# Kernel optimization log

Measured on AMD Instinct MI355X. Metric: run time of the kernel, lower is better.

## Reference

```python
import jax, jax.numpy as jnp
import numpy as np
import math

B = 2; SEQ = 4096; D_MODEL = 768; D_STATE = 128; D_CONV = 4; EXPAND = 2; HEAD_DIM = 64
D_INNER = EXPAND * D_MODEL; D_SSM = D_INNER; NH = D_SSM // HEAD_DIM  # 24 heads
CONV_DIM = D_SSM + 2 * D_STATE; CHUNK = 256
D_IN_PROJ = 2 * D_INNER + 2 * D_STATE + NH


def causal_conv1d(x, w, b):
    # x: [B, C, L]; w: [C, W] depthwise kernel; left-pad for causality; silu activation
    W = w.shape[-1]; L = x.shape[-1]
    xp = jnp.pad(x, ((0, 0), (0, 0), (W - 1, 0)))
    y = b[None, :, None] + sum(xp[:, :, k:k + L] * w[None, :, k, None] for k in range(W))
    return jax.nn.silu(y)


def segsum(a):
    # a: [..., S] -> [..., S, S]; entry (i,j) = sum_{k=j+1..i} a_k for i>=j, -inf above diag
    S = a.shape[-1]
    cs = jnp.cumsum(a, -1)
    d = cs[..., :, None] - cs[..., None, :]
    mask = jnp.tril(jnp.ones((S, S), bool))
    return jnp.where(mask, d, -jnp.inf)


def ssd_chunk_scan(x, dt, A, Bm, Cm, Dp, chunk):
    # Mamba2 SSD chunked selective scan. x:[b,l,h,p] dt:[b,l,h] A:[h] Bm,Cm:[b,l,n] Dp:[h]
    b, l, h, p = x.shape; n = Bm.shape[-1]; nc = l // chunk
    xc = x.reshape(b, nc, chunk, h, p)
    Bc = Bm.reshape(b, nc, chunk, n)
    Cc = Cm.reshape(b, nc, chunk, n)
    dtc = dt.reshape(b, nc, chunk, h)
    a = jnp.transpose(A[None, None, None, :] * dtc, (0, 3, 1, 2))  # [b,h,c,s]
    Acs = jnp.cumsum(a, -1)
    Lm = jnp.exp(segsum(a))  # [b,h,c,s,s] lower-triangular decay
    # intra-chunk (diagonal block) outputs
    Ydiag = jnp.einsum('bcsn,bczn,bhcsz,bczh,bczhp->bcshp', Cc, Bc, Lm, dtc, xc)
    # per-chunk end states
    decay_states = jnp.exp(Acs[..., -1:] - Acs)  # [b,h,c,s]
    states = jnp.einsum('bczn,bhcz,bczh,bczhp->bchpn', Bc, decay_states, dtc, xc)
    # inter-chunk recurrence over nc chunks (small) via scan
    decay_chunk = jnp.exp(Acs[..., -1])  # [b,h,c]
    def step(hcar, inp):
        dcy, st = inp
        return dcy[..., None, None] * hcar + st, hcar  # emit state entering chunk
    _, prev = jax.lax.scan(step, jnp.zeros_like(states[:, 0]),
                           (jnp.moveaxis(decay_chunk, -1, 0), jnp.moveaxis(states, 1, 0)))
    prev = jnp.moveaxis(prev, 0, 1)  # [b,c,h,p,n]
    Yoff = jnp.einsum('bcsn,bchpn,bhcs->bcshp', Cc, prev, jnp.exp(Acs))
    return (Ydiag + Yoff).reshape(b, l, h, p) + Dp[None, None, :, None] * x


def _forward(u, time_diff, W_in, b_in, conv_w, conv_b, tconv1_w, tconv1_b,
             tconv2_w, tconv2_b, mlp_w1, mlp_b1, mlp_w2, mlp_b2, gate_w, gate_b,
             ln_w, ln_b, A_log, dt_bias, Dp, norm_w, W_out, b_out):
    silu = jax.nn.silu
    zxbcdt = u @ W_in.T + b_in  # [B,L,d_in_proj], d_mlp=0
    z = zxbcdt[..., :D_SSM]
    xBC = zxbcdt[..., D_SSM:D_SSM + CONV_DIM]
    dt = zxbcdt[..., D_SSM + CONV_DIM:]  # [B,L,H]
    A = -jnp.exp(A_log)
    xBC = jnp.transpose(causal_conv1d(jnp.transpose(xBC, (0, 2, 1)), conv_w, conv_b), (0, 2, 1))
    # time-gated dt path (time_diff: [B,H,L])
    ts = silu(time_diff @ mlp_w1.T + mlp_b1) @ mlp_w2.T + mlp_b2
    tdt = ts * time_diff
    tdt = causal_conv1d(tdt, tconv1_w, tconv1_b)
    tdt = causal_conv1d(tdt, tconv2_w, tconv2_b)  # [B,H,L]
    final_dt = dt * jnp.transpose(tdt, (0, 2, 1))
    x = xBC[..., :D_SSM]
    Bm = xBC[..., D_SSM:D_SSM + D_STATE]
    Cm = xBC[..., D_SSM + D_STATE:]
    dt_sp = jax.nn.softplus(final_dt + dt_bias)
    xh = x.reshape(x.shape[0], x.shape[1], NH, HEAD_DIM)
    y = ssd_chunk_scan(xh, dt_sp, A, Bm, Cm, Dp, CHUNK).reshape(x.shape[0], x.shape[1], D_SSM)
    # gated RMSNorm (norm_before_gate=False): gate first, then normalize
    yg = y * silu(z)
    y = yg * jax.lax.rsqrt(jnp.mean(yg * yg, -1, keepdims=True) + 1e-12) * norm_w
    out = y @ W_out.T + b_out
    # time residual gate + LayerNorm over seq_len
    tg = jax.nn.sigmoid(time_diff @ gate_w.T + gate_b)  # [B,H,1]
    tmix = tg * time_diff + (1.0 - tg) * tdt
    mu = jnp.mean(tmix, -1, keepdims=True)
    var = jnp.mean((tmix - mu) ** 2, -1, keepdims=True)
    time_out = (tmix - mu) * jax.lax.rsqrt(var + 1e-12) * ln_w + ln_b
    return out, time_out


def setup_inputs():
    key = jax.random.key(0)
    ks = jax.random.split(key, 16)
    def nrm(k, shape, scale=0.02):
        return jax.random.normal(k, shape, jnp.float32) * scale
    dtv = jnp.exp(jax.random.uniform(ks[10], (NH,), jnp.float32) * (math.log(0.1) - math.log(0.001)) + math.log(0.001))
    dtv = jnp.clip(dtv, 1e-4)
    dt_bias = dtv + jnp.log(-jnp.expm1(-dtv))
    A_log = jnp.log(jax.random.uniform(ks[11], (NH,), jnp.float32, 1.0, 16.0))
    return dict(
        u=jax.random.normal(ks[0], (B, SEQ, D_MODEL), jnp.float32),
        time_diff=jax.random.uniform(ks[1], (B, NH, SEQ), jnp.float32),
        W_in=nrm(ks[2], (D_IN_PROJ, D_MODEL)), b_in=jnp.zeros((D_IN_PROJ,), jnp.float32),
        conv_w=nrm(ks[3], (CONV_DIM, D_CONV), 0.2), conv_b=jnp.zeros((CONV_DIM,), jnp.float32),
        tconv1_w=nrm(ks[4], (NH, D_CONV), 0.2), tconv1_b=jnp.zeros((NH,), jnp.float32),
        tconv2_w=nrm(ks[5], (NH, D_CONV), 0.2), tconv2_b=jnp.zeros((NH,), jnp.float32),
        mlp_w1=nrm(ks[6], (SEQ, SEQ)), mlp_b1=jnp.zeros((SEQ,), jnp.float32),
        mlp_w2=nrm(ks[7], (SEQ, SEQ)), mlp_b2=jnp.zeros((SEQ,), jnp.float32),
        gate_w=nrm(ks[8], (1, SEQ)), gate_b=jnp.zeros((1,), jnp.float32),
        ln_w=jnp.ones((SEQ,), jnp.float32), ln_b=jnp.zeros((SEQ,), jnp.float32),
        A_log=A_log, dt_bias=dt_bias, Dp=jnp.ones((NH,), jnp.float32),
        norm_w=jnp.ones((D_SSM,), jnp.float32),
        W_out=nrm(ks[9], (D_MODEL, D_INNER)), b_out=jnp.zeros((D_MODEL,), jnp.float32),
    )


def reference(u, time_diff, W_in, b_in, conv_w, conv_b, tconv1_w, tconv1_b,
              tconv2_w, tconv2_b, mlp_w1, mlp_b1, mlp_w2, mlp_b2, gate_w, gate_b,
              ln_w, ln_b, A_log, dt_bias, Dp, norm_w, W_out, b_out):
    return _forward(u, time_diff, W_in, b_in, conv_w, conv_b, tconv1_w, tconv1_b,
                    tconv2_w, tconv2_b, mlp_w1, mlp_b1, mlp_w2, mlp_b2, gate_w, gate_b,
                    ln_w, ln_b, A_log, dt_bias, Dp, norm_w, W_out, b_out)
```

## Files before the change

kernel.cpp:

```cpp
#include <hip/hip_runtime.h>
#include <math.h>

#define BB 2
#define SEQ 4096
#define DMODEL 768
#define DSTATE 128
#define NHH 24
#define HDIM 64
#define DSSM 1536
#define CDIM 1792
#define CHK 256
#define NC 16
#define DPROJ 3352
#define MR (BB*SEQ)
#define KSPLIT 32
#define XSTR 1920
#define CT 16
#define SXS 270
#define STS 134

typedef __attribute__((ext_vector_type(8))) short bf16x8;
typedef __attribute__((ext_vector_type(8))) unsigned short u16x8;
typedef __attribute__((ext_vector_type(4))) float f32x4;

__device__ __forceinline__ float siluf(float x) { return x / (1.0f + expf(-x)); }

__device__ __forceinline__ unsigned short f2bf(float f) {
    unsigned u = __float_as_uint(f);
    unsigned r = (u + 0x7fffu + ((u >> 16) & 1u)) >> 16;
    return (unsigned short)r;
}

__device__ __forceinline__ float bf2f(unsigned short u) {
    return __uint_as_float(((unsigned)u) << 16);
}

__device__ __forceinline__ float4 bf2f4(ushort4 v) {
    float4 o;
    o.x = bf2f(v.x); o.y = bf2f(v.y); o.z = bf2f(v.z); o.w = bf2f(v.w);
    return o;
}

__device__ __forceinline__ void gload_lds16(const void* g, void* l) {
    __builtin_amdgcn_global_load_lds((const __attribute__((address_space(1))) unsigned int*)g,
                                     (__attribute__((address_space(3))) unsigned int*)l, 16, 0, 0);
}

__global__ __launch_bounds__(256) void cvt_bf16_k(const float* __restrict__ in,
    unsigned short* __restrict__ out, int n_valid, int n_total)
{
    int i = (blockIdx.x * 256 + threadIdx.x) * 4;
    if (i >= n_total) return;
    ushort4 o;
    if (i + 3 < n_valid) {
        float4 v = *(const float4*)&in[i];
        o.x = f2bf(v.x); o.y = f2bf(v.y); o.z = f2bf(v.z); o.w = f2bf(v.w);
    } else {
        o.x = (i + 0 < n_valid) ? f2bf(in[i + 0]) : 0;
        o.y = (i + 1 < n_valid) ? f2bf(in[i + 1]) : 0;
        o.z = (i + 2 < n_valid) ? f2bf(in[i + 2]) : 0;
        o.w = (i + 3 < n_valid) ? f2bf(in[i + 3]) : 0;
    }
    *(ushort4*)&out[i] = o;
}

__global__ __launch_bounds__(256) void gemm_mfma_nt(
    const unsigned short* __restrict__ A, const unsigned short* __restrict__ B,
    const float* __restrict__ bias, void* __restrict__ C, int N, int K, int KT,
    int nbias, int store_bf16, int NT)
{
    __shared__ unsigned short SMEM[16384];
    const int tid = threadIdx.x;
    const int w = tid >> 6, l = tid & 63;
    const int wr = w >> 1, wc = w & 1;
    const int lr = l & 15, lk = l >> 4;
    int nwg = gridDim.x, bid = blockIdx.x;
    int wg = (nwg & 7) ? bid : ((bid & 7) * (nwg >> 3) + (bid >> 3));
    const int m0 = (wg / NT) * 128, n0 = (wg % NT) * 128;
    f32x4 acc[4][4] = {};
    const int i16 = w * 64 + l;
    const int row0 = i16 >> 2, sl = i16 & 3;
    const size_t ga0 = (size_t)(m0 + row0) * K + sl * 8;
    const size_t ga1 = (size_t)(m0 + row0 + 64) * K + sl * 8;
    const size_t gb0 = (size_t)(n0 + row0) * K + sl * 8;
    const size_t gb1 = (size_t)(n0 + row0 + 64) * K + sl * 8;
    const int lo0 = (w * 64) * 8;
    const int lo1 = (256 + w * 64) * 8;

#define STAGE(bb, kt) { int ko = (kt) * 32;                                  \
      gload_lds16(A + ga0 + ko, &SMEM[(bb) * 4096 + lo0]);                   \
      gload_lds16(A + ga1 + ko, &SMEM[(bb) * 4096 + lo1]);                   \
      gload_lds16(B + gb0 + ko, &SMEM[8192 + (bb) * 4096 + lo0]);            \
      gload_lds16(B + gb1 + ko, &SMEM[8192 + (bb) * 4096 + lo1]); }

    STAGE(0, 0);
    for (int kt = 0; kt < KT; ++kt) {
        int cur = kt & 1;
        asm volatile("s_waitcnt vmcnt(0)" ::: "memory");
        __syncthreads();
        if (kt + 1 < KT) STAGE(cur ^ 1, kt + 1);
        bf16x8 af[4], bg[4];
#pragma unroll
        for (int mi = 0; mi < 4; ++mi)
            af[mi] = *(const bf16x8*)&SMEM[cur * 4096 + (wr * 64 + mi * 16 + lr) * 32 + lk * 8];
#pragma unroll
        for (int nj = 0; nj < 4; ++nj)
            bg[nj] = *(const bf16x8*)&SMEM[8192 + cur * 4096 + (wc * 64 + nj * 16 + lr) * 32 + lk * 8];
#pragma unroll
        for (int mi = 0; mi < 4; ++mi)
#pragma unroll
            for (int nj = 0; nj < 4; ++nj)
                acc[mi][nj] = __builtin_amdgcn_mfma_f32_16x16x32_bf16(af[mi], bg[nj], acc[mi][nj], 0, 0, 0);
    }
#undef STAGE
    if (store_bf16) {
        unsigned short* CL = SMEM;
#pragma unroll
        for (int half = 0; half < 2; ++half) {
            __syncthreads();
            if (wr == half) {
#pragma unroll
                for (int nj = 0; nj < 4; ++nj) {
                    int col = n0 + wc * 64 + nj * 16 + lr;
                    float bz = (col < nbias) ? bias[col] : 0.f;
                    int cl = wc * 64 + nj * 16 + lr;
#pragma unroll
                    for (int mi = 0; mi < 4; ++mi)
#pragma unroll
                        for (int r = 0; r < 4; ++r)
                            CL[(mi * 16 + lk * 4 + r) * 136 + cl] = f2bf(acc[mi][nj][r] + bz);
                }
            }
            __syncthreads();
            for (int i = tid; i < 1024; i += 256) {
                int rr = i >> 4, c8 = (i & 15) * 8;
                int m = m0 + half * 64 + rr;
                *(u16x8*)&((unsigned short*)C)[(size_t)m * N + n0 + c8] = *(const u16x8*)&CL[rr * 136 + c8];
            }
        }
    } else {
#pragma unroll
        for (int nj = 0; nj < 4; ++nj) {
            int col = n0 + wc * 64 + nj * 16 + lr;
            float bz = (col < nbias) ? bias[col] : 0.f;
#pragma unroll
            for (int mi = 0; mi < 4; ++mi) {
#pragma unroll
                for (int r = 0; r < 4; ++r) {
                    int m = m0 + wr * 64 + mi * 16 + lk * 4 + r;
                    ((float*)C)[(size_t)m * N + col] = acc[mi][nj][r] + bz;
                }
            }
        }
    }
}

__global__ __launch_bounds__(256) void gemm_mfma_dual(
    const unsigned short* __restrict__ A,
    const unsigned short* __restrict__ B1, const float* __restrict__ bias1,
    unsigned short* __restrict__ C1, int N1, int NT1, int nbias1, int NWG1,
    const unsigned short* __restrict__ B2, const float* __restrict__ bias2,
    unsigned short* __restrict__ C2, int N2, int NT2, int nbias2,
    int K, int KT)
{
    __shared__ unsigned short SMEM[16384];
    const int tid = threadIdx.x;
    const int w = tid >> 6, l = tid & 63;
    const int wr = w >> 1, wc = w & 1;
    const int lr = l & 15, lk = l >> 4;
    int nwg = gridDim.x, bid = blockIdx.x;
    int wg = (nwg & 7) ? bid : ((bid & 7) * (nwg >> 3) + (bid >> 3));
    const unsigned short* B;
    const float* bias;
    unsigned short* C;
    int N, NT, nbias;
    if (wg < NWG1) { B = B1; bias = bias1; C = C1; N = N1; NT = NT1; nbias = nbias1; }
    else { wg -= NWG1; B = B2; bias = bias2; C = C2; N = N2; NT = NT2; nbias = nbias2; }
    const int m0 = (wg / NT) * 128, n0 = (wg % NT) * 128;
    f32x4 acc[4][4] = {};
    const int i16 = w * 64 + l;
    const int row0 = i16 >> 2, sl = i16 & 3;
    const size_t ga0 = (size_t)(m0 + row0) * K + sl * 8;
    const size_t ga1 = (size_t)(m0 + row0 + 64) * K + sl * 8;
    const size_t gb0 = (size_t)(n0 + row0) * K + sl * 8;
    const size_t gb1 = (size_t)(n0 + row0 + 64) * K + sl * 8;
    const int lo0 = (w * 64) * 8;
    const int lo1 = (256 + w * 64) * 8;

#define STAGE(bb, kt) { int ko = (kt) * 32;                                  \
      gload_lds16(A + ga0 + ko, &SMEM[(bb) * 4096 + lo0]);                   \
      gload_lds16(A + ga1 + ko, &SMEM[(bb) * 4096 + lo1]);                   \
      gload_lds16(B + gb0 + ko, &SMEM[8192 + (bb) * 4096 + lo0]);            \
      gload_lds16(B + gb1 + ko, &SMEM[8192 + (bb) * 4096 + lo1]); }

    STAGE(0, 0);
    for (int kt = 0; kt < KT; ++kt) {
        int cur = kt & 1;
        asm volatile("s_waitcnt vmcnt(0)" ::: "memory");
        __syncthreads();
        if (kt + 1 < KT) STAGE(cur ^ 1, kt + 1);
        bf16x8 af[4], bg[4];
#pragma unroll
        for (int mi = 0; mi < 4; ++mi)
            af[mi] = *(const bf16x8*)&SMEM[cur * 4096 + (wr * 64 + mi * 16 + lr) * 32 + lk * 8];
#pragma unroll
        for (int nj = 0; nj < 4; ++nj)
            bg[nj] = *(const bf16x8*)&SMEM[8192 + cur * 4096 + (wc * 64 + nj * 16 + lr) * 32 + lk * 8];
#pragma unroll
        for (int mi = 0; mi < 4; ++mi)
#pragma unroll
            for (int nj = 0; nj < 4; ++nj)
                acc[mi][nj] = __builtin_amdgcn_mfma_f32_16x16x32_bf16(af[mi], bg[nj], acc[mi][nj], 0, 0, 0);
    }
#undef STAGE
    {
        unsigned short* CL = SMEM;
#pragma unroll
        for (int half = 0; half < 2; ++half) {
            __syncthreads();
            if (wr == half) {
#pragma unroll
                for (int nj = 0; nj < 4; ++nj) {
                    int col = n0 + wc * 64 + nj * 16 + lr;
                    float bz = (col < nbias) ? bias[col] : 0.f;
                    int cl = wc * 64 + nj * 16 + lr;
#pragma unroll
                    for (int mi = 0; mi < 4; ++mi)
#pragma unroll
                        for (int r = 0; r < 4; ++r)
                            CL[(mi * 16 + lk * 4 + r) * 136 + cl] = f2bf(acc[mi][nj][r] + bz);
                }
            }
            __syncthreads();
            for (int i = tid; i < 1024; i += 256) {
                int rr = i >> 4, c8 = (i & 15) * 8;
                int m = m0 + half * 64 + rr;
                *(u16x8*)&C[(size_t)m * N + n0 + c8] = *(const u16x8*)&CL[rr * 136 + c8];
            }
        }
    }
}

__global__ __launch_bounds__(256) void gemm_skinny_nt(const float* __restrict__ A,
    const float* __restrict__ Bw, float* __restrict__ part, int N, int K)
{
    __shared__ float sA[48 * 33];
    __shared__ float sB[128 * 33];
    const int nb = blockIdx.x, kb = blockIdx.y;
    const int n0 = nb * 128;
    const int KS = K / KSPLIT;
    const int k0 = kb * KS;
    const int tid = threadIdx.x;
    const int tx = tid & 31, ty = tid >> 5;
    float acc[6][4] = {{0.f}};
    for (int kc = 0; kc < KS; kc += 32) {
        if (kc) __syncthreads();
        for (int i = tid; i < 384; i += 256) {
            int m = i >> 3, k4 = (i & 7) * 4;
            float4 v = *(const float4*)&A[(size_t)m * K + k0 + kc + k4];
            sA[m * 33 + k4 + 0] = v.x;
            sA[m * 33 + k4 + 1] = v.y;
            sA[m * 33 + k4 + 2] = v.z;
            sA[m * 33 + k4 + 3] = v.w;
        }
        for (int i = tid; i < 1024; i += 256) {
            int n = i >> 3, k4 = (i & 7) * 4;
            float4 v = *(const float4*)&Bw[(size_t)(n0 + n) * K + k0 + kc + k4];
            sB[n * 33 + k4 + 0] = v.x;
            sB[n * 33 + k4 + 1] = v.y;
            sB[n * 33 + k4 + 2] = v.z;
            sB[n * 33 + k4 + 3] = v.w;
        }
        __syncthreads();
#pragma unroll 8
        for (int kk = 0; kk < 32; ++kk) {
            float a[6], b[4];
#pragma unroll
            for (int r = 0; r < 6; ++r) a[r] = sA[(ty * 6 + r) * 33 + kk];
#pragma unroll
            for (int j = 0; j < 4; ++j) b[j] = sB[(tx + j * 32) * 33 + kk];
#pragma unroll
            for (int r = 0; r < 6; ++r)
#pragma unroll
                for (int j = 0; j < 4; ++j)
                    acc[r][j] = fmaf(a[r], b[j], acc[r][j]);
        }
    }
    float* pb = part + (size_t)kb * 48 * N;
#pragma unroll
    for (int r = 0; r < 6; ++r)
#pragma unroll
        for (int j = 0; j < 4; ++j)
            pb[(size_t)(ty * 6 + r) * N + n0 + tx + j * 32] = acc[r][j];
}

__global__ __launch_bounds__(256) void reduce_part_k(const float* __restrict__ part,
    const float* __restrict__ bias, float* __restrict__ out, int N, int act)
{
    int idx = blockIdx.x * 256 + threadIdx.x;
    if (idx >= 48 * N) return;
    int n = idx % N;
    float s = bias[n];
#pragma unroll
    for (int kb = 0; kb < KSPLIT; ++kb) s += part[(size_t)kb * 48 * N + idx];
    if (act) s = siluf(s);
    out[idx] = s;
}

__global__ __launch_bounds__(256) void conv_xbc_k(const unsigned short* __restrict__ xbc,
    const float* __restrict__ cw, const float* __restrict__ cb,
    unsigned short* __restrict__ out)
{
    int idx = blockIdx.x * 256 + threadIdx.x;
    if (idx >= 448 * (MR / CT)) return;
    int slot = idx % 448;
    int g = idx / 448;
    int c4 = slot * 4;
    int b = g / (SEQ / CT);
    int t0 = (g % (SEQ / CT)) * CT;
    size_t rb = (size_t)b * SEQ;
    float4 cw0 = *(const float4*)&cw[(c4 + 0) * 4];
    float4 cw1 = *(const float4*)&cw[(c4 + 1) * 4];
    float4 cw2 = *(const float4*)&cw[(c4 + 2) * 4];
    float4 cw3 = *(const float4*)&cw[(c4 + 3) * 4];
    float4 cbv = *(const float4*)&cb[c4];
    float4 zero = {0.f, 0.f, 0.f, 0.f};
    float4 w0, w1, w2;
    w0 = (t0 - 3 >= 0) ? bf2f4(*(const ushort4*)&xbc[(rb + t0 - 3) * XSTR + c4]) : zero;
    w1 = (t0 - 2 >= 0) ? bf2f4(*(const ushort4*)&xbc[(rb + t0 - 2) * XSTR + c4]) : zero;
    w2 = (t0 - 1 >= 0) ? bf2f4(*(const ushort4*)&xbc[(rb + t0 - 1) * XSTR + c4]) : zero;
#pragma unroll
    for (int i = 0; i < CT; ++i) {
        int t = t0 + i;
        float4 w3 = bf2f4(*(const ushort4*)&xbc[(rb + t) * XSTR + c4]);
        float a0 = cbv.x + w0.x * cw0.x + w1.x * cw0.y + w2.x * cw0.z + w3.x * cw0.w;
        float a1 = cbv.y + w0.y * cw1.x + w1.y * cw1.y + w2.y * cw1.z + w3.y * cw1.w;
        float a2 = cbv.z + w0.z * cw2.x + w1.z * cw2.y + w2.z * cw2.z + w3.z * cw2.w;
        float a3 = cbv.w + w0.w * cw3.x + w1.w * cw3.y + w2.w * cw3.z + w3.w * cw3.w;
        ushort4 o;
        o.x = f2bf(siluf(a0)); o.y = f2bf(siluf(a1));
        o.z = f2bf(siluf(a2)); o.w = f2bf(siluf(a3));
        *(ushort4*)&out[(rb + t) * CDIM + c4] = o;
        w0 = w1; w1 = w2; w2 = w3;
    }
}

__global__ __launch_bounds__(256) void time_conv_k(const float* __restrict__ ts,
    const float* __restrict__ td, const float* __restrict__ w1, const float* __restrict__ b1,
    const float* __restrict__ w2, const float* __restrict__ b2, float* __restrict__ tdt)
{
    __shared__ float u0[SEQ];
    __shared__ float u1[SEQ];
    int row = blockIdx.x, h = row % NHH;
    const float* tsr = ts + (size_t)row * SEQ;
    const float* tdr = td + (size_t)row * SEQ;
    for (int i = threadIdx.x; i < SEQ; i += 256) u0[i] = tsr[i] * tdr[i];
    __syncthreads();
    float wa[4], wb[4];
#pragma unroll
    for (int k = 0; k < 4; ++k) { wa[k] = w1[h * 4 + k]; wb[k] = w2[h * 4 + k]; }
    float ba = b1[h], bbv = b2[h];
    for (int i = threadIdx.x; i < SEQ; i += 256) {
        float acc = ba;
#pragma unroll
        for (int k = 0; k < 4; ++k) { int tt = i + k - 3; if (tt >= 0) acc = fmaf(u0[tt], wa[k], acc); }
        u1[i] = siluf(acc);
    }
    __syncthreads();
    for (int i = threadIdx.x; i < SEQ; i += 256) {
        float acc = bbv;
#pragma unroll
        for (int k = 0; k < 4; ++k) { int tt = i + k - 3; if (tt >= 0) acc = fmaf(u1[tt], wb[k], acc); }
        tdt[(size_t)row * SEQ + i] = siluf(acc);
    }
}

__global__ __launch_bounds__(256) void dtsp_cum_k(const unsigned short* __restrict__ r1,
    const float* __restrict__ tdt, const float* __restrict__ dt_bias,
    const float* __restrict__ A_log, float* __restrict__ dtp, float* __restrict__ acs)
{
    __shared__ float wsum[4];
    int blk = blockIdx.x;
    int c = blk % NC;
    int bh = blk / NC;
    int h = bh % NHH, b = bh / NHH;
    int tid = threadIdx.x;
    int s = c * CHK + tid;
    size_t base = (size_t)bh * SEQ + s;
    float x = bf2f(r1[((size_t)(b * SEQ + s)) * XSTR + CDIM + h]) * tdt[base] + dt_bias[h];
    float dt = (x > 20.0f) ? x : log1pf(expf(x));
    dtp[base] = dt;
    float Ah = -expf(A_log[h]);
    float v = Ah * dt;
    int ln = tid & 63;
#pragma unroll
    for (int off = 1; off < 64; off <<= 1) {
        float t = __shfl_up(v, off, 64);
        if (ln >= off) v += t;
    }
    if (ln == 63) wsum[tid >> 6] = v;
    __syncthreads();
    float add = 0.f;
    int wv = tid >> 6;
#pragma unroll
    for (int i = 0; i < 3; ++i)
        if (i < wv) add += wsum[i];
    acs[base] = v + add;
}

__global__ __launch_bounds__(256) void ssd_states_sraw_k(const unsigned short* __restrict__ xc,
    const float* __restrict__ dtp, const float* __restrict__ acs_g,
    float* __restrict__ st, unsigned short* __restrict__ sraw)
{
    __shared__ float s_coef[256];
    __shared__ unsigned short SXT[64 * STS];
    __shared__ unsigned short SBT[128 * STS];
    int bid = blockIdx.x;
    int blk = (gridDim.x & 7) ? bid : ((bid & 7) * (gridDim.x >> 3) + (bid >> 3));
    int tid = threadIdx.x;
    int w = tid >> 6, l = tid & 63;
    int lr = l & 15, lk = l >> 4;
    if (blk >= BB * NC * NHH) {
        int t = blk - BB * NC * NHH;
        int bc = t / 10, tile = t % 10;
        int rem = tile, st_i = 0;
        for (st_i = 0; ; ++st_i) { if (rem < st_i + 1) break; rem -= st_i + 1; }
        int zt = rem;
// ... 199 lines not shown
            for (int r = 0; r < 4; ++r) {
                float es = esw[mi][r];
#pragma unroll
                for (int nj = 0; nj < 2; ++nj)
                    acc[mi][nj][r] += es * tmp[mi][nj][r];
            }
    }
    {
        f32x4 tmp[4][2] = {};
#pragma unroll
        for (int kt = 0; kt < 4; ++kt) {
            bf16x8 av[4], bv[2];
#pragma unroll
            for (int mi = 0; mi < 4; ++mi)
                av[mi] = *(const bf16x8*)&xc[(rowbase + w * 64 + mi * 16 + lr) * CDIM + DSSM + DSTATE + kt * 32 + lk * 8];
#pragma unroll
            for (int nj = 0; nj < 2; ++nj)
                bv[nj] = *(const bf16x8*)&pvbase[(pbase + nj * 16 + lr) * DSTATE + kt * 32 + lk * 8];
#pragma unroll
            for (int mi = 0; mi < 4; ++mi)
#pragma unroll
                for (int nj = 0; nj < 2; ++nj)
                    tmp[mi][nj] = __builtin_amdgcn_mfma_f32_16x16x32_bf16(av[mi], bv[nj], tmp[mi][nj], 0, 0, 0);
        }
        float eoff = expf(az0w);
#pragma unroll
        for (int mi = 0; mi < 4; ++mi)
#pragma unroll
            for (int r = 0; r < 4; ++r) {
                float es = esw[mi][r] * eoff;
#pragma unroll
                for (int nj = 0; nj < 2; ++nj)
                    acc[mi][nj][r] += es * tmp[mi][nj][r];
            }
    }
    float dph = Dp[h];
#pragma unroll
    for (int mi = 0; mi < 4; ++mi) {
#pragma unroll
        for (int r = 0; r < 4; ++r) {
            int s = w * 64 + mi * 16 + lk * 4 + r;
#pragma unroll
            for (int nj = 0; nj < 2; ++nj) {
                int p = pbase + nj * 16 + lr;
                float xv = bf2f(xc[(rowbase + s) * CDIM + h * HDIM + p]);
                Ybf[(rowbase + s) * DSSM + h * HDIM + p] = f2bf(acc[mi][nj][r] + dph * xv);
            }
        }
    }
}

__global__ __launch_bounds__(256) void rmsnorm_k(const unsigned short* __restrict__ Ybf_in,
    const unsigned short* __restrict__ zbf, const float* __restrict__ nw,
    unsigned short* __restrict__ Ybf_out)
{
    __shared__ float red[8];
    int row = blockIdx.x;
    const unsigned short* y = Ybf_in + (size_t)row * DSSM;
    const unsigned short* z = zbf + (size_t)row * DSSM;
    float v[6];
    float ss = 0.f;
#pragma unroll
    for (int k = 0; k < 6; ++k) {
        int i = threadIdx.x + k * 256;
        float g = bf2f(y[i]) * siluf(bf2f(z[i]));
        v[k] = g;
        ss = fmaf(g, g, ss);
    }
#pragma unroll
    for (int o = 32; o > 0; o >>= 1) ss += __shfl_down(ss, o, 64);
    int wv = threadIdx.x >> 6, ln = threadIdx.x & 63;
    if (ln == 0) red[wv] = ss;
    __syncthreads();
    float tot = red[0] + red[1] + red[2] + red[3];
    float sc = rsqrtf(tot / (float)DSSM + 1e-12f);
    unsigned short* yo = Ybf_out + (size_t)row * DSSM;
#pragma unroll
    for (int k = 0; k < 6; ++k) {
        int i = threadIdx.x + k * 256;
        yo[i] = f2bf(v[k] * sc * nw[i]);
    }
}

__global__ __launch_bounds__(256) void timeout_k(const float* __restrict__ td,
    const float* __restrict__ tdt, const float* __restrict__ gw, const float* __restrict__ gb,
    const float* __restrict__ lnw, const float* __restrict__ lnb, float* __restrict__ out2)
{
    __shared__ float tm[SEQ];
    __shared__ float red[8];
    int row = blockIdx.x;
    const float* tdr = td + (size_t)row * SEQ;
    const float* tdtr = tdt + (size_t)row * SEQ;
    int wv = threadIdx.x >> 6, ln = threadIdx.x & 63;
    float part = 0.f;
    for (int i = threadIdx.x; i < SEQ; i += 256) part = fmaf(tdr[i], gw[i], part);
#pragma unroll
    for (int o = 32; o > 0; o >>= 1) part += __shfl_down(part, o, 64);
    if (ln == 0) red[wv] = part;
    __syncthreads();
    float dot = red[0] + red[1] + red[2] + red[3];
    float tg = 1.f / (1.f + expf(-(dot + gb[0])));
    __syncthreads();
    float sum = 0.f;
    for (int i = threadIdx.x; i < SEQ; i += 256) {
        float x = tg * tdr[i] + (1.f - tg) * tdtr[i];
        tm[i] = x;
        sum += x;
    }
#pragma unroll
    for (int o = 32; o > 0; o >>= 1) sum += __shfl_down(sum, o, 64);
    if (ln == 0) red[wv] = sum;
    __syncthreads();
    float mu = (red[0] + red[1] + red[2] + red[3]) / (float)SEQ;
    __syncthreads();
    float s2 = 0.f;
    for (int i = threadIdx.x; i < SEQ; i += 256) { float d = tm[i] - mu; s2 = fmaf(d, d, s2); }
#pragma unroll
    for (int o = 32; o > 0; o >>= 1) s2 += __shfl_down(s2, o, 64);
    if (ln == 0) red[wv] = s2;
    __syncthreads();
    float var = (red[0] + red[1] + red[2] + red[3]) / (float)SEQ;
    float inv = rsqrtf(var + 1e-12f);
    for (int i = threadIdx.x; i < SEQ; i += 256)
        out2[(size_t)row * SEQ + i] = (tm[i] - mu) * inv * lnw[i] + lnb[i];
}

extern "C" void kernel_launch(void* const* d_in, const int* in_sizes, int n_in,
                              void* d_out, int out_size, void* d_ws, size_t ws_size,
                              hipStream_t stream)
{
    const float* u      = (const float*)d_in[0];
    const float* td     = (const float*)d_in[1];
    const float* W_in   = (const float*)d_in[2];
    const float* b_in   = (const float*)d_in[3];
    const float* conv_w = (const float*)d_in[4];
    const float* conv_b = (const float*)d_in[5];
    const float* t1w    = (const float*)d_in[6];
    const float* t1b    = (const float*)d_in[7];
    const float* t2w    = (const float*)d_in[8];
    const float* t2b    = (const float*)d_in[9];
    const float* m1w    = (const float*)d_in[10];
    const float* m1b    = (const float*)d_in[11];
    const float* m2w    = (const float*)d_in[12];
    const float* m2b    = (const float*)d_in[13];
    const float* gw     = (const float*)d_in[14];
    const float* gb     = (const float*)d_in[15];
    const float* lnw    = (const float*)d_in[16];
    const float* lnb    = (const float*)d_in[17];
    const float* A_log  = (const float*)d_in[18];
    const float* dt_bias= (const float*)d_in[19];
    const float* Dpv    = (const float*)d_in[20];
    const float* nw     = (const float*)d_in[21];
    const float* W_out  = (const float*)d_in[22];
    const float* b_out  = (const float*)d_in[23];
    float* out  = (float*)d_out;
    float* out2 = out + (size_t)MR * DMODEL;

    float* ws = (float*)d_ws;
    size_t o = 0;
    float* zbuf  = ws + o; o += (size_t)MR * DSSM;
    float* r1    = ws + o; o += (size_t)MR * DSSM;
    float* xcv   = ws + o; o += (size_t)MR * CDIM / 2;
    float* hid   = ws + o; o += (size_t)BB * NHH * SEQ;
    float* tss   = ws + o; o += (size_t)BB * NHH * SEQ;
    float* tdt   = ws + o; o += (size_t)BB * NHH * SEQ;
    float* dtp   = ws + o; o += (size_t)MR * NHH;
    float* acs_g = ws + o; o += (size_t)MR * NHH;
    float* pvb   = ws + o; o += (size_t)BB * NC * NHH * HDIM * DSTATE;
    unsigned short* sraw = (unsigned short*)(ws + o); o += (size_t)BB * NC * 16 * 4096 / 2;
    unsigned short* r1b = (unsigned short*)r1;
    float* stb = r1;
    unsigned short* ybf16 = (unsigned short*)r1;
    float* partb = xcv;
    unsigned short* xcv_bf = (unsigned short*)xcv;
    unsigned short* u_bf  = (unsigned short*)pvb;
    unsigned short* Wi_bf = (unsigned short*)(pvb + 3145728);
    unsigned short* pv16  = (unsigned short*)pvb;
    unsigned short* zbf   = (unsigned short*)zbuf;
    unsigned short* Y_bf  = (unsigned short*)xcv;
    unsigned short* Wo_bf = (unsigned short*)(zbuf + 6291456);

    dim3 blk(256);
    gemm_skinny_nt<<<dim3(SEQ / 128, KSPLIT), blk, 0, stream>>>(td, m1w, partb, SEQ, SEQ);
    reduce_part_k<<<dim3((48 * SEQ + 255) / 256), blk, 0, stream>>>(partb, m1b, hid, SEQ, 1);
    gemm_skinny_nt<<<dim3(SEQ / 128, KSPLIT), blk, 0, stream>>>(hid, m2w, partb, SEQ, SEQ);
    reduce_part_k<<<dim3((48 * SEQ + 255) / 256), blk, 0, stream>>>(partb, m2b, tss, SEQ, 0);
    time_conv_k<<<dim3(BB * NHH), blk, 0, stream>>>(tss, td, t1w, t1b, t2w, t2b, tdt);
    cvt_bf16_k<<<dim3((MR * DMODEL / 4 + 255) / 256), blk, 0, stream>>>(u, u_bf, MR * DMODEL, MR * DMODEL);
    cvt_bf16_k<<<dim3((3456 * DMODEL / 4 + 255) / 256), blk, 0, stream>>>(W_in, Wi_bf, DPROJ * DMODEL, 3456 * DMODEL);
    gemm_mfma_dual<<<dim3((XSTR / 128) * (MR / 128) + (DSSM / 128) * (MR / 128)), blk, 0, stream>>>(
        u_bf,
        Wi_bf + (size_t)DSSM * DMODEL, b_in + DSSM, r1b, XSTR, XSTR / 128, DPROJ - DSSM, (XSTR / 128) * (MR / 128),
        Wi_bf, b_in, zbf, DSSM, DSSM / 128, DSSM,
        DMODEL, DMODEL / 32);
    conv_xbc_k<<<dim3((448 * (MR / CT) + 255) / 256), blk, 0, stream>>>(r1b, conv_w, conv_b, xcv_bf);
    dtsp_cum_k<<<dim3(BB * NHH * NC), blk, 0, stream>>>(r1b, tdt, dt_bias, A_log, dtp, acs_g);
    ssd_states_sraw_k<<<dim3(BB * NC * NHH + BB * NC * 10), blk, 0, stream>>>(xcv_bf, dtp, acs_g, stb, sraw);
    ssd_scan_k<<<dim3(BB * NHH), blk, 0, stream>>>(stb, acs_g, pv16);
    ssd_y2_k<<<dim3(BB * NC * NHH * 2), blk, 0, stream>>>(xcv_bf, dtp, acs_g, sraw, pv16, Dpv, ybf16);
    rmsnorm_k<<<dim3(MR), blk, 0, stream>>>(ybf16, zbf, nw, Y_bf);
    cvt_bf16_k<<<dim3((DMODEL * DSSM / 4 + 255) / 256), blk, 0, stream>>>(W_out, Wo_bf, DMODEL * DSSM, DMODEL * DSSM);
    gemm_mfma_nt<<<dim3((DMODEL / 128) * (MR / 128)), blk, 0, stream>>>(
        Y_bf, Wo_bf, b_out, out, DMODEL, DSSM, DSSM / 32, DMODEL, 0, DMODEL / 128);
    timeout_k<<<dim3(BB * NHH), blk, 0, stream>>>(td, tdt, gw, gb, lnw, lnb, out2);
}
```

Measured before the change: 377.7 us.

## Merge independent kernels into shared launches to overlap skinny MLP GEMMs

The first skinny time-MLP GEMM now runs as extra workgroups inside the dual input-projection GEMM launch. The second skinny GEMM is merged into the causal conv launch, and the timeout LayerNorm rows are merged into the output GEMM launch. The partial-sum buffer moves to its own workspace region so it no longer aliases xcv. The intent is to overlap small, under-occupying kernels with larger ones and cut launch count. The cost is larger shared-memory allocations for some blocks and heterogeneous blocks within one grid.

```diff
diff --git a/kernel.cpp b/kernel.cpp
--- a/kernel.cpp
+++ b/kernel.cpp
@@ -64,112 +64,71 @@
     *(ushort4*)&out[i] = o;
 }
 
-__global__ __launch_bounds__(256) void gemm_mfma_nt(
-    const unsigned short* __restrict__ A, const unsigned short* __restrict__ B,
-    const float* __restrict__ bias, void* __restrict__ C, int N, int K, int KT,
-    int nbias, int store_bf16, int NT)
-{
-    __shared__ unsigned short SMEM[16384];
-    const int tid = threadIdx.x;
-    const int w = tid >> 6, l = tid & 63;
-    const int wr = w >> 1, wc = w & 1;
-    const int lr = l & 15, lk = l >> 4;
-    int nwg = gridDim.x, bid = blockIdx.x;
-    int wg = (nwg & 7) ? bid : ((bid & 7) * (nwg >> 3) + (bid >> 3));
-    const int m0 = (wg / NT) * 128, n0 = (wg % NT) * 128;
-    f32x4 acc[4][4] = {};
-    const int i16 = w * 64 + l;
-    const int row0 = i16 >> 2, sl = i16 & 3;
-    const size_t ga0 = (size_t)(m0 + row0) * K + sl * 8;
-    const size_t ga1 = (size_t)(m0 + row0 + 64) * K + sl * 8;
-    const size_t gb0 = (size_t)(n0 + row0) * K + sl * 8;
-    const size_t gb1 = (size_t)(n0 + row0 + 64) * K + sl * 8;
-    const int lo0 = (w * 64) * 8;
-    const int lo1 = (256 + w * 64) * 8;
-
-#define STAGE(bb, kt) { int ko = (kt) * 32;                                  \
-      gload_lds16(A + ga0 + ko, &SMEM[(bb) * 4096 + lo0]);                   \
-      gload_lds16(A + ga1 + ko, &SMEM[(bb) * 4096 + lo1]);                   \
-      gload_lds16(B + gb0 + ko, &SMEM[8192 + (bb) * 4096 + lo0]);            \
-      gload_lds16(B + gb1 + ko, &SMEM[8192 + (bb) * 4096 + lo1]); }
-
-    STAGE(0, 0);
-    for (int kt = 0; kt < KT; ++kt) {
-        int cur = kt & 1;
-        asm volatile("s_waitcnt vmcnt(0)" ::: "memory");
-        __syncthreads();
-        if (kt + 1 < KT) STAGE(cur ^ 1, kt + 1);
-        bf16x8 af[4], bg[4];
-#pragma unroll
-        for (int mi = 0; mi < 4; ++mi)
-            af[mi] = *(const bf16x8*)&SMEM[cur * 4096 + (wr * 64 + mi * 16 + lr) * 32 + lk * 8];
-#pragma unroll
-        for (int nj = 0; nj < 4; ++nj)
-            bg[nj] = *(const bf16x8*)&SMEM[8192 + cur * 4096 + (wc * 64 + nj * 16 + lr) * 32 + lk * 8];
-#pragma unroll
-        for (int mi = 0; mi < 4; ++mi)
-#pragma unroll
-            for (int nj = 0; nj < 4; ++nj)
-                acc[mi][nj] = __builtin_amdgcn_mfma_f32_16x16x32_bf16(af[mi], bg[nj], acc[mi][nj], 0, 0, 0);
-    }
-#undef STAGE
-    if (store_bf16) {
-        unsigned short* CL = SMEM;
-#pragma unroll
-        for (int half = 0; half < 2; ++half) {
-            __syncthreads();
-            if (wr == half) {
-#pragma unroll
-                for (int nj = 0; nj < 4; ++nj) {
-                    int col = n0 + wc * 64 + nj * 16 + lr;
-                    float bz = (col < nbias) ? bias[col] : 0.f;
-                    int cl = wc * 64 + nj * 16 + lr;
-#pragma unroll
-                    for (int mi = 0; mi < 4; ++mi)
-#pragma unroll
-                        for (int r = 0; r < 4; ++r)
-                            CL[(mi * 16 + lk * 4 + r) * 136 + cl] = f2bf(acc[mi][nj][r] + bz);
-                }
-            }
-            __syncthreads();
-            for (int i = tid; i < 1024; i += 256) {
-                int rr = i >> 4, c8 = (i & 15) * 8;
-                int m = m0 + half * 64 + rr;
-                *(u16x8*)&((unsigned short*)C)[(size_t)m * N + n0 + c8] = *(const u16x8*)&CL[rr * 136 + c8];
-            }
-        }
-    } else {
-#pragma unroll
-        for (int nj = 0; nj < 4; ++nj) {
-            int col = n0 + wc * 64 + nj * 16 + lr;
-            float bz = (col < nbias) ? bias[col] : 0.f;
-#pragma unroll
-            for (int mi = 0; mi < 4; ++mi) {
-#pragma unroll
-                for (int r = 0; r < 4; ++r) {
-                    int m = m0 + wr * 64 + mi * 16 + lk * 4 + r;
-                    ((float*)C)[(size_t)m * N + col] = acc[mi][nj][r] + bz;
-                }
-            }
-        }
-    }
-}
-
-__global__ __launch_bounds__(256) void gemm_mfma_dual(
+__global__ __launch_bounds__(256) void gemm_dual_skinny(
     const unsigned short* __restrict__ A,
     const unsigned short* __restrict__ B1, const float* __restrict__ bias1,
     unsigned short* __restrict__ C1, int N1, int NT1, int nbias1, int NWG1,
     const unsigned short* __restrict__ B2, const float* __restrict__ bias2,
     unsigned short* __restrict__ C2, int N2, int NT2, int nbias2,
-    int K, int KT)
-{
-    __shared__ unsigned short SMEM[16384];
+    int K, int KT, int NWGD,
+    const float* __restrict__ skA, const float* __restrict__ skB,
+    float* __restrict__ skPart, int skN, int skK)
+{
+    __shared__ __align__(16) unsigned char SMEMRAW[32768];
+    unsigned short* SMEM = (unsigned short*)SMEMRAW;
     const int tid = threadIdx.x;
+    int nwg = gridDim.x, bid = blockIdx.x;
+    int wg = (nwg & 7) ? bid : ((bid & 7) * (nwg >> 3) + (bid >> 3));
+    if (wg >= NWGD) {
+        float* sA = (float*)SMEMRAW;
+        float* sB = (float*)(SMEMRAW + 48 * 33 * 4);
+        int t = wg - NWGD;
+        int nb = t & 31, kb = t >> 5;
+        const int n0 = nb * 128;
+        const int KS = skK / KSPLIT;
+        const int k0 = kb * KS;
+        const int tx = tid & 31, ty = tid >> 5;
+        float acc[6][4] = {{0.f}};
+        for (int kc = 0; kc < KS; kc += 32) {
+            if (kc) __syncthreads();
+            for (int i = tid; i < 384; i += 256) {
+                int m = i >> 3, k4 = (i & 7) * 4;
+                float4 v = *(const float4*)&skA[(size_t)m * skK + k0 + kc + k4];
+                sA[m * 33 + k4 + 0] = v.x; sA[m * 33 + k4 + 1] = v.y;
+                sA[m * 33 + k4 + 2] = v.z; sA[m * 33 + k4 + 3] = v.w;
+            }
+            for (int i = tid; i < 1024; i += 256) {
+                int n = i >> 3, k4 = (i & 7) * 4;
+                float4 v = *(const float4*)&skB[(size_t)(n0 + n) * skK + k0 + kc + k4];
+                sB[n * 33 + k4 + 0] = v.x; sB[n * 33 + k4 + 1] = v.y;
+                sB[n * 33 + k4 + 2] = v.z; sB[n * 33 + k4 + 3] = v.w;
+            }
+            __syncthreads();
+#pragma unroll 8
+            for (int kk = 0; kk < 32; ++kk) {
+                float a[6], b[4];
+#pragma unroll
+                for (int r = 0; r < 6; ++r) a[r] = sA[(ty * 6 + r) * 33 + kk];
+#pragma unroll
+                for (int j = 0; j < 4; ++j) b[j] = sB[(tx + j * 32) * 33 + kk];
+#pragma unroll
+                for (int r = 0; r < 6; ++r)
+#pragma unroll
+                    for (int j = 0; j < 4; ++j)
+                        acc[r][j] = fmaf(a[r], b[j], acc[r][j]);
+            }
+        }
+        float* pb = skPart + (size_t)kb * 48 * skN;
+#pragma unroll
+        for (int r = 0; r < 6; ++r)
+#pragma unroll
+            for (int j = 0; j < 4; ++j)
+                pb[(size_t)(ty * 6 + r) * skN + n0 + tx + j * 32] = acc[r][j];
+        return;
+    }
     const int w = tid >> 6, l = tid & 63;
     const int wr = w >> 1, wc = w & 1;
     const int lr = l & 15, lk = l >> 4;
-    int nwg = gridDim.x, bid = blockIdx.x;
-    int wg = (nwg & 7) ? bid : ((bid & 7) * (nwg >> 3) + (bid >> 3));
     const unsigned short* B;
     const float* bias;
     unsigned short* C;
@@ -187,18 +146,18 @@
     const int lo0 = (w * 64) * 8;
     const int lo1 = (256 + w * 64) * 8;
 
-#define STAGE(bb, kt) { int ko = (kt) * 32;                                  \
+#define STAGE1(bb, kt) { int ko = (kt) * 32;                                 \
       gload_lds16(A + ga0 + ko, &SMEM[(bb) * 4096 + lo0]);                   \
       gload_lds16(A + ga1 + ko, &SMEM[(bb) * 4096 + lo1]);                   \
       gload_lds16(B + gb0 + ko, &SMEM[8192 + (bb) * 4096 + lo0]);            \
       gload_lds16(B + gb1 + ko, &SMEM[8192 + (bb) * 4096 + lo1]); }
 
-    STAGE(0, 0);
+    STAGE1(0, 0);
     for (int kt = 0; kt < KT; ++kt) {
         int cur = kt & 1;
         asm volatile("s_waitcnt vmcnt(0)" ::: "memory");
         __syncthreads();
-        if (kt + 1 < KT) STAGE(cur ^ 1, kt + 1);
+        if (kt + 1 < KT) STAGE1(cur ^ 1, kt + 1);
         bf16x8 af[4], bg[4];
 #pragma unroll
         for (int mi = 0; mi < 4; ++mi)
@@ -212,7 +171,7 @@
             for (int nj = 0; nj < 4; ++nj)
                 acc[mi][nj] = __builtin_amdgcn_mfma_f32_16x16x32_bf16(af[mi], bg[nj], acc[mi][nj], 0, 0, 0);
     }
-#undef STAGE
+#undef STAGE1
     {
         unsigned short* CL = SMEM;
 #pragma unroll
@@ -241,78 +200,63 @@
     }
 }
 
-__global__ __launch_bounds__(256) void gemm_skinny_nt(const float* __restrict__ A,
-    const float* __restrict__ Bw, float* __restrict__ part, int N, int K)
-{
-    __shared__ float sA[48 * 33];
-    __shared__ float sB[128 * 33];
-    const int nb = blockIdx.x, kb = blockIdx.y;
-    const int n0 = nb * 128;
-    const int KS = K / KSPLIT;
-    const int k0 = kb * KS;
-    const int tid = threadIdx.x;
-    const int tx = tid & 31, ty = tid >> 5;
-    float acc[6][4] = {{0.f}};
-    for (int kc = 0; kc < KS; kc += 32) {
-        if (kc) __syncthreads();
-        for (int i = tid; i < 384; i += 256) {
-            int m = i >> 3, k4 = (i & 7) * 4;
-            float4 v = *(const float4*)&A[(size_t)m * K + k0 + kc + k4];
-            sA[m * 33 + k4 + 0] = v.x;
-            sA[m * 33 + k4 + 1] = v.y;
-            sA[m * 33 + k4 + 2] = v.z;
-            sA[m * 33 + k4 + 3] = v.w;
-        }
-        for (int i = tid; i < 1024; i += 256) {
-            int n = i >> 3, k4 = (i & 7) * 4;
-            float4 v = *(const float4*)&Bw[(size_t)(n0 + n) * K + k0 + kc + k4];
-            sB[n * 33 + k4 + 0] = v.x;
-            sB[n * 33 + k4 + 1] = v.y;
-            sB[n * 33 + k4 + 2] = v.z;
-            sB[n * 33 + k4 + 3] = v.w;
-        }
-        __syncthreads();
+__global__ __launch_bounds__(256) void conv_skinny_k(const unsigned short* __restrict__ xbc,
+    const float* __restrict__ cw, const float* __restrict__ cb,
+    unsigned short* __restrict__ out,
+    const float* __restrict__ skA, const float* __restrict__ skB,
+    float* __restrict__ skPart, int skN, int skK, int NWGC)
+{
+    __shared__ __align__(16) unsigned char SMEMRAW[23232];
+    int bid = blockIdx.x;
+    int tid = threadIdx.x;
+    if (bid >= NWGC) {
+        float* sA = (float*)SMEMRAW;
+        float* sB = (float*)(SMEMRAW + 48 * 33 * 4);
+        int t = bid - NWGC;
+        int nb = t & 31, kb = t >> 5;
+        const int n0 = nb * 128;
+        const int KS = skK / KSPLIT;
+        const int k0 = kb * KS;
+        const int tx = tid & 31, ty = tid >> 5;
+        float acc[6][4] = {{0.f}};
+        for (int kc = 0; kc < KS; kc += 32) {
+            if (kc) __syncthreads();
+            for (int i = tid; i < 384; i += 256) {
+                int m = i >> 3, k4 = (i & 7) * 4;
+                float4 v = *(const float4*)&skA[(size_t)m * skK + k0 + kc + k4];
+                sA[m * 33 + k4 + 0] = v.x; sA[m * 33 + k4 + 1] = v.y;
+                sA[m * 33 + k4 + 2] = v.z; sA[m * 33 + k4 + 3] = v.w;
+            }
+            for (int i = tid; i < 1024; i += 256) {
+                int n = i >> 3, k4 = (i & 7) * 4;
+                float4 v = *(const float4*)&skB[(size_t)(n0 + n) * skK + k0 + kc + k4];
+                sB[n * 33 + k4 + 0] = v.x; sB[n * 33 + k4 + 1] = v.y;
+                sB[n * 33 + k4 + 2] = v.z; sB[n * 33 + k4 + 3] = v.w;
+            }
+            __syncthreads();
 #pragma unroll 8
-        for (int kk = 0; kk < 32; ++kk) {
-            float a[6], b[4];
-#pragma unroll
-            for (int r = 0; r < 6; ++r) a[r] = sA[(ty * 6 + r) * 33 + kk];
-#pragma unroll
-            for (int j = 0; j < 4; ++j) b[j] = sB[(tx + j * 32) * 33 + kk];
-#pragma unroll
-            for (int r = 0; r < 6; ++r)
-#pragma unroll
-                for (int j = 0; j < 4; ++j)
-                    acc[r][j] = fmaf(a[r], b[j], acc[r][j]);
-        }
-    }
-    float* pb = part + (size_t)kb * 48 * N;
-#pragma unroll
-    for (int r = 0; r < 6; ++r)
-#pragma unroll
-        for (int j = 0; j < 4; ++j)
-            pb[(size_t)(ty * 6 + r) * N + n0 + tx + j * 32] = acc[r][j];
-}
-
-__global__ __launch_bounds__(256) void reduce_part_k(const float* __restrict__ part,
-    const float* __restrict__ bias, float* __restrict__ out, int N, int act)
-{
-    int idx = blockIdx.x * 256 + threadIdx.x;
-    if (idx >= 48 * N) return;
-    int n = idx % N;
-    float s = bias[n];
-#pragma unroll
-    for (int kb = 0; kb < KSPLIT; ++kb) s += part[(size_t)kb * 48 * N + idx];
-    if (act) s = siluf(s);
-    out[idx] = s;
-}
-
-__global__ __launch_bounds__(256) void conv_xbc_k(const unsigned short* __restrict__ xbc,
-    const float* __restrict__ cw, const float* __restrict__ cb,
-    unsigned short* __restrict__ out)
-{
-    int idx = blockIdx.x * 256 + threadIdx.x;
-    if (idx >= 448 * (MR / CT)) return;
+            for (int kk = 0; kk < 32; ++kk) {
+                float a[6], b[4];
+#pragma unroll
+                for (int r = 0; r < 6; ++r) a[r] = sA[(ty * 6 + r) * 33 + kk];
+#pragma unroll
+                for (int j = 0; j < 4; ++j) b[j] = sB[(tx + j * 32) * 33 + kk];
+#pragma unroll
+                for (int r = 0; r < 6; ++r)
+#pragma unroll
+                    for (int j = 0; j < 4; ++j)
+                        acc[r][j] = fmaf(a[r], b[j], acc[r][j]);
+            }
+        }
+        float* pb = skPart + (size_t)kb * 48 * skN;
+#pragma unroll
+        for (int r = 0; r < 6; ++r)
+#pragma unroll
+            for (int j = 0; j < 4; ++j)
+                pb[(size_t)(ty * 6 + r) * skN + n0 + tx + j * 32] = acc[r][j];
+        return;
+    }
+    int idx = bid * 256 + tid;
     int slot = idx % 448;
     int g = idx / 448;
     int c4 = slot * 4;
@@ -343,6 +287,19 @@
         *(ushort4*)&out[(rb + t) * CDIM + c4] = o;
         w0 = w1; w1 = w2; w2 = w3;
     }
+}
+
+__global__ __launch_bounds__(256) void reduce_part_k(const float* __restrict__ part,
+    const float* __restrict__ bias, float* __restrict__ out, int N, int act)
+{
+    int idx = blockIdx.x * 256 + threadIdx.x;
+    if (idx >= 48 * N) return;
+    int n = idx % N;
+    float s = bias[n];
+#pragma unroll
+    for (int kb = 0; kb < KSPLIT; ++kb) s += part[(size_t)kb * 48 * N + idx];
+    if (act) s = siluf(s);
+    out[idx] = s;
 }
 
 __global__ __launch_bounds__(256) void time_conv_k(const float* __restrict__ ts,
@@ -708,47 +665,111 @@
     }
 }
 
-__global__ __launch_bounds__(256) void timeout_k(const float* __restrict__ td,
-    const float* __restrict__ tdt, const float* __restrict__ gw, const float* __restrict__ gb,
+__global__ __launch_bounds__(256) void gemm_out_timeout_k(
+    const unsigned short* __restrict__ A, const unsigned short* __restrict__ B,
+    const float* __restrict__ bias, float* __restrict__ C, int N, int K, int KT, int NT, int NWGG,
+    const float* __restrict__ td, const float* __restrict__ tdt,
+    const float* __restrict__ gw, const float* __restrict__ gb,
     const float* __restrict__ lnw, const float* __restrict__ lnb, float* __restrict__ out2)
 {
-    __shared__ float tm[SEQ];
-    __shared__ float red[8];
-    int row = blockIdx.x;
-    const float* tdr = td + (size_t)row * SEQ;
-    const float* tdtr = tdt + (size_t)row * SEQ;
-    int wv = threadIdx.x >> 6, ln = threadIdx.x & 63;
-    float part = 0.f;
-    for (int i = threadIdx.x; i < SEQ; i += 256) part = fmaf(tdr[i], gw[i], part);
-#pragma unroll
-    for (int o = 32; o > 0; o >>= 1) part += __shfl_down(part, o, 64);
-    if (ln == 0) red[wv] = part;
-    __syncthreads();
-    float dot = red[0] + red[1] + red[2] + red[3];
-    float tg = 1.f / (1.f + expf(-(dot + gb[0])));
-    __syncthreads();
-    float sum = 0.f;
-    for (int i = threadIdx.x; i < SEQ; i += 256) {
-        float x = tg * tdr[i] + (1.f - tg) * tdtr[i];
-        tm[i] = x;
-        sum += x;
-    }
-#pragma unroll
-    for (int o = 32; o > 0; o >>= 1) sum += __shfl_down(sum, o, 64);
-    if (ln == 0) red[wv] = sum;
-    __syncthreads();
-    float mu = (red[0] + red[1] + red[2] + red[3]) / (float)SEQ;
-    __syncthreads();
-    float s2 = 0.f;
-    for (int i = threadIdx.x; i < SEQ; i += 256) { float d = tm[i] - mu; s2 = fmaf(d, d, s2); }
-#pragma unroll
-    for (int o = 32; o > 0; o >>= 1) s2 += __shfl_down(s2, o, 64);
-    if (ln == 0) red[wv] = s2;
-    __syncthreads();
-    float var = (red[0] + red[1] + red[2] + red[3]) / (float)SEQ;
-    float inv = rsqrtf(var + 1e-12f);
-    for (int i = threadIdx.x; i < SEQ; i += 256)
-        out2[(size_t)row * SEQ + i] = (tm[i] - mu) * inv * lnw[i] + lnb[i];
+    __shared__ __align__(16) unsigned char SMEMRAW[32768];
+    unsigned short* SMEM = (unsigned short*)SMEMRAW;
+    const int tid = threadIdx.x;
+    int nwg = gridDim.x, bid = blockIdx.x;
+    int wg = (nwg & 7) ? bid : ((bid & 7) * (nwg >> 3) + (bid >> 3));
+    if (wg >= NWGG) {
+        float* tm = (float*)SMEMRAW;
+        __shared__ float red[8];
+        int row = wg - NWGG;
+        const float* tdr = td + (size_t)row * SEQ;
+        const float* tdtr = tdt + (size_t)row * SEQ;
+        int wv = tid >> 6, ln = tid & 63;
+        float part = 0.f;
+        for (int i = tid; i < SEQ; i += 256) part = fmaf(tdr[i], gw[i], part);
+#pragma unroll
+        for (int o = 32; o > 0; o >>= 1) part += __shfl_down(part, o, 64);
+        if (ln == 0) red[wv] = part;
+        __syncthreads();
+        float dot = red[0] + red[1] + red[2] + red[3];
+        float tg = 1.f / (1.f + expf(-(dot + gb[0])));
+        __syncthreads();
+        float sum = 0.f;
+        for (int i = tid; i < SEQ; i += 256) {
+            float x = tg * tdr[i] + (1.f - tg) * tdtr[i];
+            tm[i] = x;
+            sum += x;
+        }
+#pragma unroll
+        for (int o = 32; o > 0; o >>= 1) sum += __shfl_down(sum, o, 64);
+        if (ln == 0) red[wv] = sum;
+        __syncthreads();
+        float mu = (red[0] + red[1] + red[2] + red[3]) / (float)SEQ;
+        __syncthreads();
+        float s2 = 0.f;
+        for (int i = tid; i < SEQ; i += 256) { float d = tm[i] - mu; s2 = fmaf(d, d, s2); }
+#pragma unroll
+        for (int o = 32; o > 0; o >>= 1) s2 += __shfl_down(s2, o, 64);
+        if (ln == 0) red[wv] = s2;
+        __syncthreads();
+        float var = (red[0] + red[1] + red[2] + red[3]) / (float)SEQ;
+        float inv = rsqrtf(var + 1e-12f);
+        for (int i = tid; i < SEQ; i += 256)
+            out2[(size_t)row * SEQ + i] = (tm[i] - mu) * inv * lnw[i] + lnb[i];
+        return;
+    }
+    const int w = tid >> 6, l = tid & 63;
+    const int wr = w >> 1, wc = w & 1;
+    const int lr = l & 15, lk = l >> 4;
+    const int m0 = (wg / NT) * 128, n0 = (wg % NT) * 128;
+    f32x4 acc[4][4] = {};
+    const int i16 = w * 64 + l;
+    const int row0 = i16 >> 2, sl = i16 & 3;
+    const size_t ga0 = (size_t)(m0 + row0) * K + sl * 8;
+    const size_t ga1 = (size_t)(m0 + row0 + 64) * K + sl * 8;
+    const size_t gb0 = (size_t)(n0 + row0) * K + sl * 8;
+    const size_t gb1 = (size_t)(n0 + row0 + 64) * K + sl * 8;
+    const int lo0 = (w * 64) * 8;
+    const int lo1 = (256 + w * 64) * 8;
+
+#define STAGE3(bb, kt) { int ko = (kt) * 32;                                 \
+      gload_lds16(A + ga0 + ko, &SMEM[(bb) * 4096 + lo0]);                   \
+      gload_lds16(A + ga1 + ko, &SMEM[(bb) * 4096 + lo1]);                   \
+      gload_lds16(B + gb0 + ko, &SMEM[8192 + (bb) * 4096 + lo0]);            \
+      gload_lds16(B + gb1 + ko, &SMEM[8192 + (bb) * 4096 + lo1]); }
+
+    STAGE3(0, 0);
+    for (int kt = 0; kt < KT; ++kt) {
+        int cur = kt & 1;
+        asm volatile("s_waitcnt vmcnt(0)" ::: "memory");
+        __syncthreads();
+        if (kt + 1 < KT) STAGE3(cur ^ 1, kt + 1);
+        bf16x8 af[4], bg[4];
+#pragma unroll
+        for (int mi = 0; mi < 4; ++mi)
+            af[mi] = *(const bf16x8*)&SMEM[cur * 4096 + (wr * 64 + mi * 16 + lr) * 32 + lk * 8];
+#pragma unroll
+        for (int nj = 0; nj < 4; ++nj)
+            bg[nj] = *(const bf16x8*)&SMEM[8192 + cur * 4096 + (wc * 64 + nj * 16 + lr) * 32 + lk * 8];
+#pragma unroll
+        for (int mi = 0; mi < 4; ++mi)
+#pragma unroll
+            for (int nj = 0; nj < 4; ++nj)
+                acc[mi][nj] = __builtin_amdgcn_mfma_f32_16x16x32_bf16(af[mi], bg[nj], acc[mi][nj], 0, 0, 0);
+    }
+#undef STAGE3
+#pragma unroll
+    for (int nj = 0; nj < 4; ++nj) {
+        int col = n0 + wc * 64 + nj * 16 + lr;
+        float bz = bias[col];
+#pragma unroll
+        for (int mi = 0; mi < 4; ++mi) {
+#pragma unroll
+            for (int r = 0; r < 4; ++r) {
+                int m = m0 + wr * 64 + mi * 16 + lk * 4 + r;
+                C[(size_t)m * N + col] = acc[mi][nj][r] + bz;
+            }
+        }
+    }
 }
 
 extern "C" void kernel_launch(void* const* d_in, const int* in_sizes, int n_in,
@@ -787,6 +808,7 @@
     float* zbuf  = ws + o; o += (size_t)MR * DSSM;
     float* r1    = ws + o; o += (size_t)MR * DSSM;
     float* xcv   = ws + o; o += (size_t)MR * CDIM / 2;
+    float* partb = ws + o; o += (size_t)KSPLIT * 48 * SEQ;
     float* hid   = ws + o; o += (size_t)BB * NHH * SEQ;
     float* tss   = ws + o; o += (size_t)BB * NHH * SEQ;
     float* tdt   = ws + o; o += (size_t)BB * NHH * SEQ;
@@ -797,7 +819,6 @@
     unsigned short* r1b = (unsigned short*)r1;
     float* stb = r1;
     unsigned short* ybf16 = (unsigned short*)r1;
-    float* partb = xcv;
     unsigned short* xcv_bf = (unsigned short*)xcv;
     unsigned short* u_bf  = (unsigned short*)pvb;
     unsigned short* Wi_bf = (unsigned short*)(pvb + 3145728);
@@ -807,26 +828,31 @@
     unsigned short* Wo_bf = (unsigned short*)(zbuf + 6291456);
 
     dim3 blk(256);
-    gemm_skinny_nt<<<dim3(SEQ / 128, KSPLIT), blk, 0, stream>>>(td, m1w, partb, SEQ, SEQ);
+    const int NWG1 = (XSTR / 128) * (MR / 128);
+    const int NWGD = NWG1 + (DSSM / 128) * (MR / 128);
+    const int NWGSK = (SEQ / 128) * KSPLIT;
+    const int NWGC = 448 * (MR / CT) / 256;
+
+    cvt_bf16_k<<<dim3((MR * DMODEL / 4 + 255) / 256), blk, 0, stream>>>(u, u_bf, MR * DMODEL, MR * DMODEL);
+    cvt_bf16_k<<<dim3((3456 * DMODEL / 4 + 255) / 256), blk, 0, stream>>>(W_in, Wi_bf, DPROJ * DMODEL, 3456 * DMODEL);
+    cvt_bf16_k<<<dim3((DMODEL * DSSM / 4 + 255) / 256), blk, 0, stream>>>(W_out, Wo_bf, DMODEL * DSSM, DMODEL * DSSM);
+    gemm_dual_skinny<<<dim3(NWGD + NWGSK), blk, 0, stream>>>(
+        u_bf,
+        Wi_bf + (size_t)DSSM * DMODEL, b_in + DSSM, r1b, XSTR, XSTR / 128, DPROJ - DSSM, NWG1,
+        Wi_bf, b_in, zbf, DSSM, DSSM / 128, DSSM,
+        DMODEL, DMODEL / 32, NWGD,
+        td, m1w, partb, SEQ, SEQ);
     reduce_part_k<<<dim3((48 * SEQ + 255) / 256), blk, 0, stream>>>(partb, m1b, hid, SEQ, 1);
-    gemm_skinny_nt<<<dim3(SEQ / 128, KSPLIT), blk, 0, stream>>>(hid, m2w, partb, SEQ, SEQ);
+    conv_skinny_k<<<dim3(NWGC + NWGSK), blk, 0, stream>>>(
+        r1b, conv_w, conv_b, xcv_bf, hid, m2w, partb, SEQ, SEQ, NWGC);
     reduce_part_k<<<dim3((48 * SEQ + 255) / 256), blk, 0, stream>>>(partb, m2b, tss, SEQ, 0);
     time_conv_k<<<dim3(BB * NHH), blk, 0, stream>>>(tss, td, t1w, t1b, t2w, t2b, tdt);
-    cvt_bf16_k<<<dim3((MR * DMODEL / 4 + 255) / 256), blk, 0, stream>>>(u, u_bf, MR * DMODEL, MR * DMODEL);
-    cvt_bf16_k<<<dim3((3456 * DMODEL / 4 + 255) / 256), blk, 0, stream>>>(W_in, Wi_bf, DPROJ * DMODEL, 3456 * DMODEL);
-    gemm_mfma_dual<<<dim3((XSTR / 128) * (MR / 128) + (DSSM / 128) * (MR / 128)), blk, 0, stream>>>(
-        u_bf,
-        Wi_bf + (size_t)DSSM * DMODEL, b_in + DSSM, r1b, XSTR, XSTR / 128, DPROJ - DSSM, (XSTR / 128) * (MR / 128),
-        Wi_bf, b_in, zbf, DSSM, DSSM / 128, DSSM,
-        DMODEL, DMODEL / 32);
-    conv_xbc_k<<<dim3((448 * (MR / CT) + 255) / 256), blk, 0, stream>>>(r1b, conv_w, conv_b, xcv_bf);
     dtsp_cum_k<<<dim3(BB * NHH * NC), blk, 0, stream>>>(r1b, tdt, dt_bias, A_log, dtp, acs_g);
     ssd_states_sraw_k<<<dim3(BB * NC * NHH + BB * NC * 10), blk, 0, stream>>>(xcv_bf, dtp, acs_g, stb, sraw);
     ssd_scan_k<<<dim3(BB * NHH), blk, 0, stream>>>(stb, acs_g, pv16);
     ssd_y2_k<<<dim3(BB * NC * NHH * 2), blk, 0, stream>>>(xcv_bf, dtp, acs_g, sraw, pv16, Dpv, ybf16);
     rmsnorm_k<<<dim3(MR), blk, 0, stream>>>(ybf16, zbf, nw, Y_bf);
-    cvt_bf16_k<<<dim3((DMODEL * DSSM / 4 + 255) / 256), blk, 0, stream>>>(W_out, Wo_bf, DMODEL * DSSM, DMODEL * DSSM);
-    gemm_mfma_nt<<<dim3((DMODEL / 128) * (MR / 128)), blk, 0, stream>>>(
-        Y_bf, Wo_bf, b_out, out, DMODEL, DSSM, DSSM / 32, DMODEL, 0, DMODEL / 128);
-    timeout_k<<<dim3(BB * NHH), blk, 0, stream>>>(td, tdt, gw, gb, lnw, lnb, out2);
-}
+    gemm_out_timeout_k<<<dim3((DMODEL / 128) * (MR / 128) + BB * NHH), blk, 0, stream>>>(
+        Y_bf, Wo_bf, b_out, out, DMODEL, DSSM, DSSM / 32, DMODEL / 128, (DMODEL / 128) * (MR / 128),
+        td, tdt, gw, gb, lnw, lnb, out2);
+}
```

Result: slower. 387.8 us (+2.7%).
